# Optimization experiments

Hardware: AMD Instinct MI355X
Metric: run time of the kernel (lower is better)

Reference implementation:

```python
import jax, jax.numpy as jnp
import numpy as np

NUM_NODES = 10000
IN_DIM = 128
GAT_UNITS = 64
K = 20  # min(20, num_nodes - 1)
NEG_SLOPE = 0.2


def setup_inputs() -> dict:
    key = jax.random.key(0)
    ks = jax.random.split(key, 10)
    s = lambda k, shape, scale: jax.random.normal(k, shape, jnp.float32) * scale
    return {
        "x": s(ks[0], (NUM_NODES, IN_DIM), 1.0),
        "emb": s(ks[1], (NUM_NODES, 16), 1.0),
        "W1": s(ks[2], (IN_DIM, 4, GAT_UNITS), 0.05),
        "a1_src": s(ks[3], (4, GAT_UNITS), 0.05),
        "a1_tgt": s(ks[4], (4, GAT_UNITS), 0.05),
        "b1": jnp.zeros((4 * GAT_UNITS,), jnp.float32),
        "W2": s(ks[5], (4 * GAT_UNITS, 1, GAT_UNITS), 0.05),
        "a2_src": s(ks[6], (1, GAT_UNITS), 0.05),
        "a2_tgt": s(ks[7], (1, GAT_UNITS), 0.05),
        "b2": jnp.zeros((GAT_UNITS,), jnp.float32),
    }


def _build_edges(emb):
    # top-k adjacency from cosine similarity of node embeddings
    norm = emb / jnp.linalg.norm(emb, axis=-1, keepdims=True)
    sim = norm @ norm.T                      # [N, N]
    _, idx = jax.lax.top_k(sim, K)           # [N, K]
    n = emb.shape[0]
    src = jnp.repeat(jnp.arange(n, dtype=jnp.int32), K)
    tgt = idx.reshape(-1).astype(jnp.int32)
    # append self loops (as in the original module)
    loop = jnp.arange(n, dtype=jnp.int32)
    src = jnp.concatenate([src, loop])
    tgt = jnp.concatenate([tgt, loop])
    return src, tgt                          # each [N*(K+1)]


def _gat(x, W, a_src, a_tgt, src, tgt, n):
    # x: [N, F]; W: [F, H, C]; a_*: [H, C]
    h = jnp.einsum("nf,fhc->nhc", x, W)      # [N, H, C]
    e_src = jnp.einsum("nhc,hc->nh", h, a_src)  # [N, H]
    e_tgt = jnp.einsum("nhc,hc->nh", h, a_tgt)  # [N, H]
    logits = jax.nn.leaky_relu(e_src[src] + e_tgt[tgt], NEG_SLOPE)  # [E, H]
    # segment softmax over each source node's neighborhood
    m = jax.ops.segment_max(logits, src, num_segments=n)
    ex = jnp.exp(logits - m[src])
    z = jax.ops.segment_sum(ex, src, num_segments=n)
    alpha = ex / z[src]                      # [E, H]
    msg = alpha[:, :, None] * h[tgt]         # [E, H, C]
    return jax.ops.segment_sum(msg, src, num_segments=n)  # [N, H, C]


def reference(x, emb, W1, a1_src, a1_tgt, b1, W2, a2_src, a2_tgt, b2):
    n = x.shape[0]
    src, tgt = _build_edges(emb)
    # GAT layer 1: 4 heads, concatenated
    h1 = _gat(x, W1, a1_src, a1_tgt, src, tgt, n)        # [N, 4, C]
    h1 = h1.reshape(n, -1) + b1                           # [N, 4C]
    h1 = jax.nn.relu(h1)                                  # (dropout: inference mode)
    # GAT layer 2: 1 head, no concat
    h2 = _gat(h1, W2, a2_src, a2_tgt, src, tgt, n)        # [N, 1, C]
    return h2[:, 0, :] + b2                               # [N, C]
```

## Files before the change

kernel.cpp:

```cpp
#include <hip/hip_runtime.h>
#include <math.h>


#define N_NODES 10000
#define EMB_D   16
#define IN_DIM  128
#define H1      4
#define CDIM    64
#define D1      256
#define K_TOP   20
#define NEIGH   21
#define SROWS   32
#define NTILES  313
#define JSPLIT  2
#define HALFT   160
#define CAPM    96
#define GUARD   0.016f

typedef __attribute__((ext_vector_type(8)))  short short8;
typedef __attribute__((ext_vector_type(16))) float f32x16;

__device__ __forceinline__ unsigned monokey(float v) {
  unsigned u = __float_as_uint(v);
  return (u & 0x80000000u) ? ~u : (u | 0x80000000u);
}
__device__ __forceinline__ float invmono(unsigned m) {
  unsigned u = (m & 0x80000000u) ? (m ^ 0x80000000u) : ~m;
  return __uint_as_float(u);
}
__device__ __forceinline__ unsigned short f32_to_bf16(float f) {
  unsigned u = __float_as_uint(f);
  unsigned r = 0x7FFFu + ((u >> 16) & 1u);
  return (unsigned short)((u + r) >> 16);
}

__device__ __forceinline__ float dot16q(float4 qa, float4 qb, float4 qc, float4 qd,
                                        float4 v0, float4 v1, float4 v2, float4 v3) {
  float a = 0.f;
  a = fmaf(qa.x, v0.x, a); a = fmaf(qa.y, v0.y, a);
  a = fmaf(qa.z, v0.z, a); a = fmaf(qa.w, v0.w, a);
  a = fmaf(qb.x, v1.x, a); a = fmaf(qb.y, v1.y, a);
  a = fmaf(qb.z, v1.z, a); a = fmaf(qb.w, v1.w, a);
  a = fmaf(qc.x, v2.x, a); a = fmaf(qc.y, v2.y, a);
  a = fmaf(qc.z, v2.z, a); a = fmaf(qc.w, v2.w, a);
  a = fmaf(qd.x, v3.x, a); a = fmaf(qd.y, v3.y, a);
  a = fmaf(qd.z, v3.z, a); a = fmaf(qd.w, v3.w, a);
  return a;
}

__global__ __launch_bounds__(256) void normalize_kernel(
    const float* __restrict__ emb, float* __restrict__ nrm,
    unsigned short* __restrict__ nrmh) {
  int i = blockIdx.x * 256 + threadIdx.x;
  if (i >= N_NODES) return;
  const float4* p = (const float4*)(emb + (size_t)i * EMB_D);
  float4 v[4];
  float ss = 0.f;
#pragma unroll
  for (int k = 0; k < 4; k++) {
    v[k] = p[k];
    ss = fmaf(v[k].x, v[k].x, ss);
    ss = fmaf(v[k].y, v[k].y, ss);
    ss = fmaf(v[k].z, v[k].z, ss);
    ss = fmaf(v[k].w, v[k].w, ss);
  }
  float nv = sqrtf(ss);
  float4* o = (float4*)(nrm + (size_t)i * EMB_D);
  ushort4* oh = (ushort4*)(nrmh + (size_t)i * EMB_D);
#pragma unroll
  for (int k = 0; k < 4; k++) {
    float4 t;
    t.x = v[k].x / nv; t.y = v[k].y / nv; t.z = v[k].z / nv; t.w = v[k].w / nv;
    o[k] = t;
    ushort4 h;
    h.x = f32_to_bf16(t.x); h.y = f32_to_bf16(t.y);
    h.z = f32_to_bf16(t.z); h.w = f32_to_bf16(t.w);
    oh[k] = h;
  }
}

__global__ __launch_bounds__(512) void sim_topk_part(
    const float* __restrict__ nrm, const unsigned short* __restrict__ nrmh,
    unsigned short* __restrict__ cids, int* __restrict__ cnts) {
  __shared__ unsigned short s_qbf[SROWS * EMB_D];
  __shared__ float s_qf[SROWS * EMB_D];
  __shared__ float s_smax[SROWS][256];
  __shared__ float s_thr[SROWS];
  __shared__ int s_cnt[SROWS];

  int tid = threadIdx.x;
  int w = tid >> 6, lane = tid & 63;
  int lo5 = lane & 31, hi = lane >> 5;
  int row0 = blockIdx.x * SROWS;
  int bh = blockIdx.y;
  int tbase = bh * HALFT;

  if (tid < SROWS * EMB_D) {
    int gi = row0 * EMB_D + tid;
    float v = (gi < N_NODES * EMB_D) ? nrm[gi] : 0.f;
    s_qf[tid] = v;
    s_qbf[tid] = f32_to_bf16(v);
  }
  if (tid < SROWS) s_cnt[tid] = 0;
  __syncthreads();

  short8 afrag = *(const short8*)&s_qbf[lo5 * EMB_D + hi * 8];
  const f32x16 zacc = (f32x16)0.0f;

  float rm[16];
#pragma unroll
  for (int r = 0; r < 16; r++) rm[r] = -INFINITY;

#pragma unroll
  for (int g = 0; g < 5; ++g) {
    int tb = tbase + g * 32 + w * 4;
    int nd[4];
    short8 bf[4];
#pragma unroll
    for (int u = 0; u < 4; u++) {
      nd[u] = (tb + u) * 32 + lo5;
      bf[u] = (short8)(short)0;
      if (nd[u] < N_NODES)
        bf[u] = *(const short8*)&nrmh[(size_t)nd[u] * EMB_D + hi * 8];
    }
#pragma unroll
    for (int u = 0; u < 4; u++) {
      f32x16 acc = __builtin_amdgcn_mfma_f32_32x32x16_bf16(afrag, bf[u], zacc, 0, 0, 0);
      if (nd[u] < N_NODES) {
#pragma unroll
        for (int r = 0; r < 16; r++) rm[r] = fmaxf(rm[r], acc[r]);
      }
    }
  }
#pragma unroll
  for (int r = 0; r < 16; r++) {
    int rl = (r & 3) + 8 * (r >> 2) + 4 * hi;
    s_smax[rl][w * 32 + lo5] = rm[r];
  }
  __syncthreads();

  for (int q = 0; q < 4; q++) {
    int row = w * 4 + q;
    float m01 = fmaxf(s_smax[row][lane], s_smax[row][64 + lane]);
    float m23 = fmaxf(s_smax[row][128 + lane], s_smax[row][192 + lane]);
    unsigned v = monokey(fmaxf(m01, m23));
#pragma unroll
    for (int k = 2; k <= 64; k <<= 1) {
#pragma unroll
      for (int j = k >> 1; j > 0; j >>= 1) {
        unsigned o = __shfl_xor(v, j);
        bool upper = (lane & j) != 0;
        bool ascend = (lane & k) == 0;
        unsigned mx = v > o ? v : o;
        unsigned mn = v > o ? o : v;
        v = (upper == ascend) ? mx : mn;
      }
    }
    unsigned t20 = __shfl(v, 44);
    if (lane == 0)
      s_thr[row] = (row0 + row < N_NODES) ? invmono(t20) - GUARD : INFINITY;
  }
  __syncthreads();

  float thr_r[16];
#pragma unroll
  for (int r = 0; r < 16; r++)
    thr_r[r] = s_thr[(r & 3) + 8 * (r >> 2) + 4 * hi];

#pragma unroll
  for (int g = 0; g < 5; ++g) {
    int tb = tbase + g * 32 + w * 4;
    int nd[4];
    short8 bf[4];
#pragma unroll
    for (int u = 0; u < 4; u++) {
      nd[u] = (tb + u) * 32 + lo5;
      bf[u] = (short8)(short)0;
      if (nd[u] < N_NODES)
        bf[u] = *(const short8*)&nrmh[(size_t)nd[u] * EMB_D + hi * 8];
    }
#pragma unroll
    for (int u = 0; u < 4; u++) {
      f32x16 acc = __builtin_amdgcn_mfma_f32_32x32x16_bf16(afrag, bf[u], zacc, 0, 0, 0);
      if (nd[u] < N_NODES) {
#pragma unroll
        for (int r = 0; r < 16; r++) {
          if (acc[r] >= thr_r[r]) {
            int rl = (r & 3) + 8 * (r >> 2) + 4 * hi;
            int slot = atomicAdd(&s_cnt[rl], 1);
            if (slot < CAPM)
              cids[((size_t)(row0 + rl) * JSPLIT + bh) * CAPM + slot] =
                  (unsigned short)nd[u];
          }
        }
      }
    }
  }
  __syncthreads();

  for (int q = 0; q < 4; q++) {
    int row = w * 4 + q;
    int grow = row0 + row;
    if (grow >= N_NODES) continue;
    int M = s_cnt[row];
    if (M <= CAPM) {
      if (lane == 0) cnts[grow * JSPLIT + bh] = M;
    } else {
      unsigned short* outc = cids + ((size_t)grow * JSPLIT + bh) * CAPM;
      const float4* qp = (const float4*)&s_qf[row * EMB_D];
      float4 qa = qp[0], qb = qp[1], qc = qp[2], qd = qp[3];
      int j0 = tbase * 32;
      int jend = j0 + HALFT * 32; if (jend > N_NODES) jend = N_NODES;
      unsigned long long prev = ~0ull;
      for (int r = 0; r < K_TOP; r++) {
        unsigned long long best = 0ull;
        for (int j = j0 + lane; j < jend; j += 64) {
          const float4* pj = (const float4*)(nrm + (size_t)j * EMB_D);
          float sim = dot16q(qa, qb, qc, qd, pj[0], pj[1], pj[2], pj[3]);
          unsigned long long key = ((unsigned long long)monokey(sim) << 32) |
                                   (unsigned long long)(0xFFFFFFFFu - (unsigned)j);
          if (key < prev && key > best) best = key;
        }
#pragma unroll
        for (int off = 32; off > 0; off >>= 1) {
          unsigned long long o = __shfl_down(best, off);
          if (o > best) best = o;
        }
        best = __shfl(best, 0);
        prev = best;
        if (lane == 0)
          outc[r] = (unsigned short)(0xFFFFFFFFu - (unsigned)(best & 0xFFFFFFFFull));
      }
      if (lane == 0) cnts[grow * JSPLIT + bh] = K_TOP;
    }
  }
}

__global__ __launch_bounds__(256) void topk_merge(
    const float* __restrict__ nrm, const unsigned short* __restrict__ cids,
    const int* __restrict__ cnts, int* __restrict__ topk) {
  __shared__ unsigned long long s_k[4][JSPLIT * CAPM];
  int w = threadIdx.x >> 6, lane = threadIdx.x & 63;
  int row = blockIdx.x * 4 + w;
  int M1 = cnts[row * JSPLIT + 0];
  int M2 = cnts[row * JSPLIT + 1];
  int M = M1 + M2;
  const float4* qp = (const float4*)(nrm + (size_t)row * EMB_D);
  float4 qa = qp[0], qb = qp[1], qc = qp[2], qd = qp[3];
  const unsigned short* c0 = cids + ((size_t)row * JSPLIT + 0) * CAPM;
  const unsigned short* c1 = cids + ((size_t)row * JSPLIT + 1) * CAPM;
  for (int c = lane; c < M; c += 64) {
    int id = (c < M1) ? c0[c] : c1[c - M1];
    const float4* pj = (const float4*)(nrm + (size_t)id * EMB_D);
    float sim = dot16q(qa, qb, qc, qd, pj[0], pj[1], pj[2], pj[3]);
    s_k[w][c] = ((unsigned long long)monokey(sim) << 32) |
                (unsigned long long)(0xFFFFFFFFu - (unsigned)id);
  }
  __syncthreads();
  for (int c = lane; c < M; c += 64) {
    unsigned long long mykey = s_k[w][c];
    int rank = 0;
    for (int i = 0; i < M; i++) rank += (s_k[w][i] > mykey) ? 1 : 0;
    if (rank < K_TOP)
      topk[(size_t)row * K_TOP + rank] =
          (int)(0xFFFFFFFFu - (unsigned)(mykey & 0xFFFFFFFFull));
  }
}

__global__ __launch_bounds__(256) void gemm1_kernel(
    const float* __restrict__ A, const float* __restrict__ B,
    const float* __restrict__ a_src, const float* __restrict__ a_tgt,
    float* __restrict__ Cc, float* __restrict__ es, float* __restrict__ et) {
  __shared__ float As[16][IN_DIM];
  int r0 = blockIdx.x * 16;
  int tid = threadIdx.x;
  {
    int rr = tid >> 4;
    int kk = tid & 15;
    ((float4*)&As[rr][0])[kk] = ((const float4*)(A + (size_t)(r0 + rr) * IN_DIM))[kk];
    ((float4*)&As[rr][0])[kk + 16] =
        ((const float4*)(A + (size_t)(r0 + rr) * IN_DIM))[kk + 16];
  }
  __syncthreads();
  int y = tid >> 7;
  int c0 = (tid & 127) * 2;
  float acc[8][2] = {};
  for (int k4 = 0; k4 < IN_DIM / 4; k4++) {
    float4 a[8];
#pragma unroll
    for (int r = 0; r < 8; r++) a[r] = ((const float4*)&As[y * 8 + r][0])[k4];
    float2 bv[4];
#pragma unroll
    for (int i = 0; i < 4; i++)
      bv[i] = *(const float2*)&B[(size_t)(k4 * 4 + i) * D1 + c0];
#pragma unroll
    for (int r = 0; r < 8; r++) {
      acc[r][0] = fmaf(a[r].x, bv[0].x, acc[r][0]);
      acc[r][1] = fmaf(a[r].x, bv[0].y, acc[r][1]);
      acc[r][0] = fmaf(a[r].y, bv[1].x, acc[r][0]);
      acc[r][1] = fmaf(a[r].y, bv[1].y, acc[r][1]);
      acc[r][0] = fmaf(a[r].z, bv[2].x, acc[r][0]);
      acc[r][1] = fmaf(a[r].z, bv[2].y, acc[r][1]);
      acc[r][0] = fmaf(a[r].w, bv[3].x, acc[r][0]);
      acc[r][1] = fmaf(a[r].w, bv[3].y, acc[r][1]);
    }
  }
#pragma unroll
  for (int r = 0; r < 8; r++) {
    float2 o = {acc[r][0], acc[r][1]};
    *(float2*)&Cc[(size_t)(r0 + y * 8 + r) * D1 + c0] = o;
  }
  int lane = tid & 63;
  int h = c0 >> 6;
  float as0 = a_src[c0], as1 = a_src[c0 + 1];
  float at0 = a_tgt[c0], at1 = a_tgt[c0 + 1];
#pragma unroll
  for (int r = 0; r < 8; r++) {
    float ps = fmaf(acc[r][1], as1, acc[r][0] * as0);
    float pt = fmaf(acc[r][1], at1, acc[r][0] * at0);
#pragma unroll
    for (int off = 16; off > 0; off >>= 1) {
      ps += __shfl_down(ps, off);
      pt += __shfl_down(pt, off);
    }
    if ((lane & 31) == 0) {
      es[(size_t)(r0 + y * 8 + r) * H1 + h] = ps;
      et[(size_t)(r0 + y * 8 + r) * H1 + h] = pt;
    }
  }
}

__global__ __launch_bounds__(256) void agg1_gemm2_kernel(
    const float* __restrict__ h1p, const float* __restrict__ e1s,
    const float* __restrict__ e1t, const int* __restrict__ topk,
    const float* __restrict__ b1, const float* __restrict__ B2,
    const float* __restrict__ a_src, const float* __restrict__ a_tgt,
    float* __restrict__ h2p, float* __restrict__ es, float* __restrict__ et) {
  __shared__ float As[16][D1];
  __shared__ int nb[16][NEIGH];
  __shared__ float wv[16][NEIGH][H1];
  __shared__ float zz[16][H1];
  int r0 = blockIdx.x * 16;
  int tid = threadIdx.x;

  for (int idx = tid; idx < 16 * NEIGH; idx += 256) {
    int n = idx / NEIGH, jj = idx % NEIGH;
    nb[n][jj] = (jj < K_TOP) ? topk[(size_t)(r0 + n) * K_TOP + jj] : (r0 + n);
  }
  __syncthreads();
  for (int idx = tid; idx < 16 * NEIGH * H1; idx += 256) {
    int e = idx & 3, jj = (idx >> 2) % NEIGH, n = idx / (NEIGH * H1);
    float L = e1s[(size_t)(r0 + n) * H1 + e] + e1t[(size_t)nb[n][jj] * H1 + e];
    wv[n][jj][e] = (L > 0.f) ? L : 0.2f * L;
  }
  __syncthreads();
  if (tid < 16 * H1) {
    int n = tid >> 2, h = tid & 3;
    float m = -INFINITY;
#pragma unroll
    for (int jj = 0; jj < NEIGH; jj++) m = fmaxf(m, wv[n][jj][h]);
    float z = 0.f;
#pragma unroll
    for (int jj = 0; jj < NEIGH; jj++) {
      float wt = expf(wv[n][jj][h] - m);
      z += wt;
      wv[n][jj][h] = wt;
    }
    zz[n][h] = z;
  }
  __syncthreads();
  {
    int h = tid >> 6;
    float bv = b1[tid];
    for (int n = 0; n < 16; n++) {
      float acc = 0.f;
#pragma unroll
      for (int jj = 0; jj < NEIGH; jj++)
        acc = fmaf(wv[n][jj][h], h1p[(size_t)nb[n][jj] * D1 + tid], acc);
      float o = acc / zz[n][h] + bv;
      As[n][tid] = fmaxf(o, 0.f);
    }
  }
  __syncthreads();
  int col = tid & 63, y = tid >> 6;
  float acc4[4] = {0, 0, 0, 0};
  for (int k4 = 0; k4 < D1 / 4; k4++) {
    float4 a[4];
#pragma unroll
    for (int r = 0; r < 4; r++) a[r] = ((const float4*)&As[y * 4 + r][0])[k4];
    float bv[4];
#pragma unroll
    for (int i = 0; i < 4; i++) bv[i] = B2[(size_t)(k4 * 4 + i) * CDIM + col];
#pragma unroll
    for (int r = 0; r < 4; r++) {
      acc4[r] = fmaf(a[r].x, bv[0], acc4[r]);
      acc4[r] = fmaf(a[r].y, bv[1], acc4[r]);
      acc4[r] = fmaf(a[r].z, bv[2], acc4[r]);
      acc4[r] = fmaf(a[r].w, bv[3], acc4[r]);
    }
  }
#pragma unroll
  for (int r = 0; r < 4; r++)
    h2p[(size_t)(r0 + y * 4 + r) * CDIM + col] = acc4[r];
  float as = a_src[col], at = a_tgt[col];
#pragma unroll
  for (int r = 0; r < 4; r++) {
    float ps = acc4[r] * as, pt = acc4[r] * at;
#pragma unroll
    for (int off = 32; off > 0; off >>= 1) {
      ps += __shfl_down(ps, off);
      pt += __shfl_down(pt, off);
    }
    if (col == 0) {
      es[r0 + y * 4 + r] = ps;
      et[r0 + y * 4 + r] = pt;
    }
  }
}

__global__ __launch_bounds__(256) void agg2_kernel(
    const float* __restrict__ h2p, const float* __restrict__ es,
    const float* __restrict__ et, const int* __restrict__ topk,
    const float* __restrict__ b2, float* __restrict__ out) {
  int tid = threadIdx.x;
  int li = tid >> 6;
  int c = tid & 63;
  int i = blockIdx.x * 4 + li;
  __shared__ int nb[4][NEIGH];
  __shared__ float lg[4][NEIGH];
  if (tid < 4 * NEIGH) {
    int li2 = tid / NEIGH, jj = tid % NEIGH;
    int node = blockIdx.x * 4 + li2;
    nb[li2][jj] = (jj < K_TOP) ? topk[(size_t)node * K_TOP + jj] : node;
  }
  __syncthreads();
  if (tid < 4 * NEIGH) {
    int li2 = tid / NEIGH, jj = tid % NEIGH;
    int node = blockIdx.x * 4 + li2;
    float L = es[node] + et[nb[li2][jj]];
    lg[li2][jj] = (L > 0.f) ? L : 0.2f * L;
  }
  __syncthreads();
  float m = -INFINITY;
#pragma unroll
  for (int jj = 0; jj < NEIGH; jj++) m = fmaxf(m, lg[li][jj]);
  float z = 0.f, acc = 0.f;
#pragma unroll
  for (int jj = 0; jj < NEIGH; jj++) {
    float w = expf(lg[li][jj] - m);
    z += w;
    acc = fmaf(w, h2p[(size_t)nb[li][jj] * CDIM + c], acc);
  }
  out[(size_t)i * CDIM + c] = acc / z + b2[c];
}

extern "C" void kernel_launch(void* const* d_in, const int* in_sizes, int n_in,
                              void* d_out, int out_size, void* d_ws, size_t ws_size,
                              hipStream_t stream) {
  const float* x   = (const float*)d_in[0];
  const float* emb = (const float*)d_in[1];
  const float* W1  = (const float*)d_in[2];
  const float* a1s = (const float*)d_in[3];
  const float* a1t = (const float*)d_in[4];
  const float* b1  = (const float*)d_in[5];
  const float* W2  = (const float*)d_in[6];
  const float* a2s = (const float*)d_in[7];
  const float* a2t = (const float*)d_in[8];
  const float* b2  = (const float*)d_in[9];
  float* out = (float*)d_out;

  size_t off = 0;
  auto alloc = [&](size_t bytes) {
    void* p = (char*)d_ws + off;
    off += (bytes + 255) & ~(size_t)255;
    return p;
  };
  float*          nrm  = (float*)alloc((size_t)N_NODES * EMB_D * sizeof(float));
  unsigned short* nrmh = (unsigned short*)alloc((size_t)N_NODES * EMB_D * sizeof(unsigned short));
  int*   topk = (int*)  alloc((size_t)N_NODES * K_TOP * sizeof(int));
  float* h1p  = (float*)alloc((size_t)N_NODES * D1 * sizeof(float));
  float* e1s  = (float*)alloc((size_t)N_NODES * H1 * sizeof(float));
  float* e1t  = (float*)alloc((size_t)N_NODES * H1 * sizeof(float));
  float* h2p  = (float*)alloc((size_t)N_NODES * CDIM * sizeof(float));
  float* e2s  = (float*)alloc((size_t)N_NODES * sizeof(float));
  float* e2t  = (float*)alloc((size_t)N_NODES * sizeof(float));
  unsigned short* cids = (unsigned short*)h1p;
  int* cnts = (int*)((char*)h1p + (size_t)N_NODES * JSPLIT * CAPM * sizeof(unsigned short));
  (void)ws_size; (void)in_sizes; (void)n_in; (void)out_size;

  normalize_kernel<<<(N_NODES + 255) / 256, 256, 0, stream>>>(emb, nrm, nrmh);
  sim_topk_part<<<dim3(NTILES, JSPLIT), 512, 0, stream>>>(nrm, nrmh, cids, cnts);
  topk_merge<<<N_NODES / 4, 256, 0, stream>>>(nrm, cids, cnts, topk);
  gemm1_kernel<<<N_NODES / 16, 256, 0, stream>>>(x, W1, a1s, a1t, h1p, e1s, e1t);
  agg1_gemm2_kernel<<<N_NODES / 16, 256, 0, stream>>>(h1p, e1s, e1t, topk, b1,
                                                      W2, a2s, a2t, h2p, e2s, e2t);
  agg2_kernel<<<N_NODES / 4, 256, 0, stream>>>(h2p, e2s, e2t, topk, b2, out);
}
```

Measured before the change: 140.5 us.

## Split similarity top-k over four column quarters and halve rows per agg1 block

The similarity/top-k candidate kernel now splits the column range into four quarters instead of two, with each wave taking a contiguous run of tiles. This doubles the grid and shortens the per-block loop, and the merge kernel is generalised to walk any number of partial candidate lists. Separately, the fused layer-1 aggregation plus layer-2 GEMM kernel now handles 8 nodes per block instead of 16, which doubles the number of blocks. Both changes aim for more parallelism and occupancy. The cost is more candidates to merge per row, more global candidate and count traffic, and less reuse of W2 per block.

```diff
diff --git a/kernel.cpp b/kernel.cpp
--- a/kernel.cpp
+++ b/kernel.cpp
@@ -12,10 +12,11 @@
 #define NEIGH   21
 #define SROWS   32
 #define NTILES  313
-#define JSPLIT  2
-#define HALFT   160
+#define JSPLIT  4
+#define QTILES  80
 #define CAPM    96
 #define GUARD   0.016f
+#define NPB     8
 
 typedef __attribute__((ext_vector_type(8)))  short short8;
 typedef __attribute__((ext_vector_type(16))) float f32x16;
@@ -92,8 +93,8 @@
   int w = tid >> 6, lane = tid & 63;
   int lo5 = lane & 31, hi = lane >> 5;
   int row0 = blockIdx.x * SROWS;
-  int bh = blockIdx.y;
-  int tbase = bh * HALFT;
+  int bq = blockIdx.y;
+  int tbase = bq * QTILES + w * (QTILES / 8);
 
   if (tid < SROWS * EMB_D) {
     int gi = row0 * EMB_D + tid;
@@ -112,19 +113,19 @@
   for (int r = 0; r < 16; r++) rm[r] = -INFINITY;
 
 #pragma unroll
-  for (int g = 0; g < 5; ++g) {
-    int tb = tbase + g * 32 + w * 4;
-    int nd[4];
-    short8 bf[4];
-#pragma unroll
-    for (int u = 0; u < 4; u++) {
+  for (int g = 0; g < 2; ++g) {
+    int tb = tbase + g * 5;
+    int nd[5];
+    short8 bf[5];
+#pragma unroll
+    for (int u = 0; u < 5; u++) {
       nd[u] = (tb + u) * 32 + lo5;
       bf[u] = (short8)(short)0;
       if (nd[u] < N_NODES)
         bf[u] = *(const short8*)&nrmh[(size_t)nd[u] * EMB_D + hi * 8];
     }
 #pragma unroll
-    for (int u = 0; u < 4; u++) {
+    for (int u = 0; u < 5; u++) {
       f32x16 acc = __builtin_amdgcn_mfma_f32_32x32x16_bf16(afrag, bf[u], zacc, 0, 0, 0);
       if (nd[u] < N_NODES) {
 #pragma unroll
@@ -168,19 +169,19 @@
     thr_r[r] = s_thr[(r & 3) + 8 * (r >> 2) + 4 * hi];
 
 #pragma unroll
-  for (int g = 0; g < 5; ++g) {
-    int tb = tbase + g * 32 + w * 4;
-    int nd[4];
-    short8 bf[4];
-#pragma unroll
-    for (int u = 0; u < 4; u++) {
+  for (int g = 0; g < 2; ++g) {
+    int tb = tbase + g * 5;
+    int nd[5];
+    short8 bf[5];
+#pragma unroll
+    for (int u = 0; u < 5; u++) {
       nd[u] = (tb + u) * 32 + lo5;
       bf[u] = (short8)(short)0;
       if (nd[u] < N_NODES)
         bf[u] = *(const short8*)&nrmh[(size_t)nd[u] * EMB_D + hi * 8];
     }
 #pragma unroll
-    for (int u = 0; u < 4; u++) {
+    for (int u = 0; u < 5; u++) {
       f32x16 acc = __builtin_amdgcn_mfma_f32_32x32x16_bf16(afrag, bf[u], zacc, 0, 0, 0);
       if (nd[u] < N_NODES) {
 #pragma unroll
@@ -189,7 +190,7 @@
             int rl = (r & 3) + 8 * (r >> 2) + 4 * hi;
             int slot = atomicAdd(&s_cnt[rl], 1);
             if (slot < CAPM)
-              cids[((size_t)(row0 + rl) * JSPLIT + bh) * CAPM + slot] =
+              cids[((size_t)(row0 + rl) * JSPLIT + bq) * CAPM + slot] =
                   (unsigned short)nd[u];
           }
         }
@@ -204,13 +205,13 @@
     if (grow >= N_NODES) continue;
     int M = s_cnt[row];
     if (M <= CAPM) {
-      if (lane == 0) cnts[grow * JSPLIT + bh] = M;
+      if (lane == 0) cnts[grow * JSPLIT + bq] = M;
     } else {
-      unsigned short* outc = cids + ((size_t)grow * JSPLIT + bh) * CAPM;
+      unsigned short* outc = cids + ((size_t)grow * JSPLIT + bq) * CAPM;
       const float4* qp = (const float4*)&s_qf[row * EMB_D];
       float4 qa = qp[0], qb = qp[1], qc = qp[2], qd = qp[3];
-      int j0 = tbase * 32;
-      int jend = j0 + HALFT * 32; if (jend > N_NODES) jend = N_NODES;
+      int j0 = bq * QTILES * 32;
+      int jend = j0 + QTILES * 32; if (jend > N_NODES) jend = N_NODES;
       unsigned long long prev = ~0ull;
       for (int r = 0; r < K_TOP; r++) {
         unsigned long long best = 0ull;
@@ -231,7 +232,7 @@
         if (lane == 0)
           outc[r] = (unsigned short)(0xFFFFFFFFu - (unsigned)(best & 0xFFFFFFFFull));
       }
-      if (lane == 0) cnts[grow * JSPLIT + bh] = K_TOP;
+      if (lane == 0) cnts[grow * JSPLIT + bq] = K_TOP;
     }
   }
 }
@@ -242,15 +243,19 @@
   __shared__ unsigned long long s_k[4][JSPLIT * CAPM];
   int w = threadIdx.x >> 6, lane = threadIdx.x & 63;
   int row = blockIdx.x * 4 + w;
-  int M1 = cnts[row * JSPLIT + 0];
-  int M2 = cnts[row * JSPLIT + 1];
-  int M = M1 + M2;
+  int Ms[JSPLIT];
+  int M = 0;
+#pragma unroll
+  for (int s = 0; s < JSPLIT; s++) {
+    Ms[s] = cnts[row * JSPLIT + s];
+    M += Ms[s];
+  }
   const float4* qp = (const float4*)(nrm + (size_t)row * EMB_D);
   float4 qa = qp[0], qb = qp[1], qc = qp[2], qd = qp[3];
-  const unsigned short* c0 = cids + ((size_t)row * JSPLIT + 0) * CAPM;
-  const unsigned short* c1 = cids + ((size_t)row * JSPLIT + 1) * CAPM;
   for (int c = lane; c < M; c += 64) {
-    int id = (c < M1) ? c0[c] : c1[c - M1];
+    int cc = c, s = 0;
+    while (cc >= Ms[s]) { cc -= Ms[s]; s++; }
+    int id = cids[((size_t)row * JSPLIT + s) * CAPM + cc];
     const float4* pj = (const float4*)(nrm + (size_t)id * EMB_D);
     float sim = dot16q(qa, qb, qc, qd, pj[0], pj[1], pj[2], pj[3]);
     s_k[w][c] = ((unsigned long long)monokey(sim) << 32) |
@@ -336,25 +341,25 @@
     const float* __restrict__ b1, const float* __restrict__ B2,
     const float* __restrict__ a_src, const float* __restrict__ a_tgt,
     float* __restrict__ h2p, float* __restrict__ es, float* __restrict__ et) {
-  __shared__ float As[16][D1];
-  __shared__ int nb[16][NEIGH];
-  __shared__ float wv[16][NEIGH][H1];
-  __shared__ float zz[16][H1];
-  int r0 = blockIdx.x * 16;
+  __shared__ float As[NPB][D1];
+  __shared__ int nb[NPB][NEIGH];
+  __shared__ float wv[NPB][NEIGH][H1];
+  __shared__ float zz[NPB][H1];
+  int r0 = blockIdx.x * NPB;
   int tid = threadIdx.x;
 
-  for (int idx = tid; idx < 16 * NEIGH; idx += 256) {
+  for (int idx = tid; idx < NPB * NEIGH; idx += 256) {
     int n = idx / NEIGH, jj = idx % NEIGH;
     nb[n][jj] = (jj < K_TOP) ? topk[(size_t)(r0 + n) * K_TOP + jj] : (r0 + n);
   }
   __syncthreads();
-  for (int idx = tid; idx < 16 * NEIGH * H1; idx += 256) {
+  for (int idx = tid; idx < NPB * NEIGH * H1; idx += 256) {
     int e = idx & 3, jj = (idx >> 2) % NEIGH, n = idx / (NEIGH * H1);
     float L = e1s[(size_t)(r0 + n) * H1 + e] + e1t[(size_t)nb[n][jj] * H1 + e];
     wv[n][jj][e] = (L > 0.f) ? L : 0.2f * L;
   }
   __syncthreads();
-  if (tid < 16 * H1) {
+  if (tid < NPB * H1) {
     int n = tid >> 2, h = tid & 3;
     float m = -INFINITY;
 #pragma unroll
@@ -372,7 +377,7 @@
   {
     int h = tid >> 6;
     float bv = b1[tid];
-    for (int n = 0; n < 16; n++) {
+    for (int n = 0; n < NPB; n++) {
       float acc = 0.f;
 #pragma unroll
       for (int jj = 0; jj < NEIGH; jj++)
@@ -383,37 +388,37 @@
   }
   __syncthreads();
   int col = tid & 63, y = tid >> 6;
-  float acc4[4] = {0, 0, 0, 0};
+  float acc2[2] = {0, 0};
   for (int k4 = 0; k4 < D1 / 4; k4++) {
-    float4 a[4];
-#pragma unroll
-    for (int r = 0; r < 4; r++) a[r] = ((const float4*)&As[y * 4 + r][0])[k4];
+    float4 a[2];
+#pragma unroll
+    for (int r = 0; r < 2; r++) a[r] = ((const float4*)&As[y * 2 + r][0])[k4];
     float bv[4];
 #pragma unroll
     for (int i = 0; i < 4; i++) bv[i] = B2[(size_t)(k4 * 4 + i) * CDIM + col];
 #pragma unroll
-    for (int r = 0; r < 4; r++) {
-      acc4[r] = fmaf(a[r].x, bv[0], acc4[r]);
-      acc4[r] = fmaf(a[r].y, bv[1], acc4[r]);
-      acc4[r] = fmaf(a[r].z, bv[2], acc4[r]);
-      acc4[r] = fmaf(a[r].w, bv[3], acc4[r]);
-    }
-  }
-#pragma unroll
-  for (int r = 0; r < 4; r++)
-    h2p[(size_t)(r0 + y * 4 + r) * CDIM + col] = acc4[r];
+    for (int r = 0; r < 2; r++) {
+      acc2[r] = fmaf(a[r].x, bv[0], acc2[r]);
+      acc2[r] = fmaf(a[r].y, bv[1], acc2[r]);
+      acc2[r] = fmaf(a[r].z, bv[2], acc2[r]);
+      acc2[r] = fmaf(a[r].w, bv[3], acc2[r]);
+    }
+  }
+#pragma unroll
+  for (int r = 0; r < 2; r++)
+    h2p[(size_t)(r0 + y * 2 + r) * CDIM + col] = acc2[r];
   float as = a_src[col], at = a_tgt[col];
 #pragma unroll
-  for (int r = 0; r < 4; r++) {
-    float ps = acc4[r] * as, pt = acc4[r] * at;
+  for (int r = 0; r < 2; r++) {
+    float ps = acc2[r] * as, pt = acc2[r] * at;
 #pragma unroll
     for (int off = 32; off > 0; off >>= 1) {
       ps += __shfl_down(ps, off);
       pt += __shfl_down(pt, off);
     }
     if (col == 0) {
-      es[r0 + y * 4 + r] = ps;
-      et[r0 + y * 4 + r] = pt;
+      es[r0 + y * 2 + r] = ps;
+      et[r0 + y * 2 + r] = pt;
     }
   }
 }
@@ -492,7 +497,7 @@
   sim_topk_part<<<dim3(NTILES, JSPLIT), 512, 0, stream>>>(nrm, nrmh, cids, cnts);
   topk_merge<<<N_NODES / 4, 256, 0, stream>>>(nrm, cids, cnts, topk);
   gemm1_kernel<<<N_NODES / 16, 256, 0, stream>>>(x, W1, a1s, a1t, h1p, e1s, e1t);
-  agg1_gemm2_kernel<<<N_NODES / 16, 256, 0, stream>>>(h1p, e1s, e1t, topk, b1,
-                                                      W2, a2s, a2t, h2p, e2s, e2t);
+  agg1_gemm2_kernel<<<N_NODES / NPB, 256, 0, stream>>>(h1p, e1s, e1t, topk, b1,
+                                                       W2, a2s, a2t, h2p, e2s, e2t);
   agg2_kernel<<<N_NODES / 4, 256, 0, stream>>>(h2p, e2s, e2t, topk, b2, out);
 }
```

Result: slower. 158.2 us (+12.6%).
